# Optimization experiments

Measured on AMD Instinct MI355X. Metric: run time of the kernel, lower is better.

The kernel has to match this reference:

```python
import jax, jax.numpy as jnp
import numpy as np

MARGIN = 1.0


def setup_inputs() -> dict:
    key = jax.random.key(0)
    k1, k2, k3 = jax.random.split(key, 3)
    B, D, C = 16384, 256, 2000
    pred_embedding = jax.random.normal(k1, (B, D), dtype=jnp.float32)
    batch_label = jax.random.randint(k2, (B,), 0, C, dtype=jnp.int64)
    train_classes = jnp.arange(C, dtype=jnp.int64)
    train_sig = jax.random.normal(k3, (D, C), dtype=jnp.float32)
    return {
        "pred_embedding": pred_embedding,
        "batch_label": batch_label,
        "train_classes": train_classes,
        "train_sig": train_sig,
    }


def reference(pred_embedding, batch_label, train_classes, train_sig):
    # scores[j, k] = <pred_embedding[j], train_sig[:, train_classes[k]]>
    # Single GEMM replaces the per-pair dot-product loops.
    sig_cols = train_sig[:, train_classes]            # [D, C]
    scores = jnp.einsum("bd,dc->bc", pred_embedding, sig_cols)  # [B, C]
    # ground-truth class score per row: <XW_j, train_sig[:, y_j]>
    gt = jnp.einsum("bd,db->b", pred_embedding, train_sig[:, batch_label])  # [B]
    # exclude the class equal to the row label
    mask = (train_classes[None, :] != batch_label[:, None])  # [B, C] bool
    hinge = jnp.maximum(MARGIN + scores - gt[:, None], 0.0)
    loss = jnp.sum(jnp.where(mask, hinge, 0.0))
    return loss
```

## Files before the change

### kernel.cpp

```cpp
#include <hip/hip_runtime.h>

#define B_SZ 16384
#define D_SZ 256
#define C_SZ 2000
#define C_PAD 2048
#define MARGIN_F 1.0f
#define NBLK 1024

typedef float floatx16 __attribute__((ext_vector_type(16)));

__device__ inline void gld_lds16(const void* g, void* l) {
  __builtin_amdgcn_global_load_lds(
      (const __attribute__((address_space(1))) void*)g,
      (__attribute__((address_space(3))) void*)l, 16, 0, 0);
}


__device__ inline int2 pack8_fp8(const float* v) {
  int lo = __builtin_amdgcn_cvt_pk_fp8_f32(v[0], v[1], 0, false);
  lo = __builtin_amdgcn_cvt_pk_fp8_f32(v[2], v[3], lo, true);
  int hi = __builtin_amdgcn_cvt_pk_fp8_f32(v[4], v[5], 0, false);
  hi = __builtin_amdgcn_cvt_pk_fp8_f32(v[6], v[7], hi, true);
  return make_int2(lo, hi);
}
__device__ inline float rt_fp8(float x) {
  int p = __builtin_amdgcn_cvt_pk_fp8_f32(x, x, 0, false);
  return __builtin_amdgcn_cvt_f32_fp8(p, 0);
}
__device__ inline void unpack4_fp8(int w, float* o) {
  o[0] = __builtin_amdgcn_cvt_f32_fp8(w, 0);
  o[1] = __builtin_amdgcn_cvt_f32_fp8(w, 1);
  o[2] = __builtin_amdgcn_cvt_f32_fp8(w, 2);
  o[3] = __builtin_amdgcn_cvt_f32_fp8(w, 3);
}

__global__ __launch_bounds__(256) void sigq_kernel(
    const float* __restrict__ sig, char* __restrict__ sigq,
    float* __restrict__ out) {
  int t = blockIdx.x * 256 + threadIdx.x;
  if (t == 0) out[0] = 0.f;
  int ln = t & 63, ks = (t >> 6) & 15, ct = t >> 10;
  int col = ct * 32 + (ln & 31);
  int kb = ks * 16 + (ln >> 5) * 8;
  float v[8];
#pragma unroll
  for (int j = 0; j < 8; j++)
    v[j] = (col < C_SZ) ? sig[(size_t)(kb + j) * C_SZ + col] : 0.f;
  *(int2*)(sigq + (size_t)t * 8) = pack8_fp8(v);
}

__global__ __launch_bounds__(256) void prep_kernel(
    const float* __restrict__ pred, const char* __restrict__ sigq,
    const int* __restrict__ label, char* __restrict__ predq,
    float* __restrict__ gt) {
  __shared__ float ldsP[16][260];
  int bid = (int)blockIdx.x;
  int tid = threadIdx.x;
  int lane = tid & 63;
  int w = tid >> 6;
  int tile = bid >> 1;
  int rhi = (bid & 1) * 16;
#pragma unroll
  for (int it = 0; it < 4; it++) {
    int idx = it * 1024 + tid * 4;
    int r = idx >> 8, c = idx & 255;
    *(float4*)&ldsP[r][c] = *(const float4*)(pred + (size_t)(bid * 16 + r) * D_SZ + c);
  }
  __syncthreads();
#pragma unroll
  for (int it = 0; it < 2; it++) {
    int ch = it * 256 + tid;
    int ri = ch & 15;
    int ks = (ch >> 4) & 15;
    int khh = ch >> 8;
    int kb = ks * 16 + khh * 8;
    int ln = khh * 32 + rhi + ri;
    float v[8];
#pragma unroll
    for (int j = 0; j < 8; j++) v[j] = ldsP[ri][kb + j];
    *(int2*)(predq + ((size_t)(tile * 16 + ks) * 64 + ln) * 8) = pack8_fp8(v);
  }
  int l = lane & 31;
  int half = lane >> 5;
#pragma unroll
  for (int it = 0; it < 2; it++) {
    int r = w * 4 + it * 2 + half;
    int row = bid * 16 + r;
    int lbl = label[row];
    int ltile = lbl >> 5, l5 = lbl & 31;
    int ks = l >> 1, khh = l & 1;
    int2 p8 = *(const int2*)(sigq +
        (((size_t)(ltile * 16 + ks) * 64) + khh * 32 + l5) * 8);
    float sv[8];
    unpack4_fp8(p8.x, sv);
    unpack4_fp8(p8.y, sv + 4);
    float s = 0.f;
#pragma unroll
    for (int j = 0; j < 8; j++)
      s += rt_fp8(ldsP[r][l * 8 + j]) * sv[j];
#pragma unroll
    for (int off = 16; off > 0; off >>= 1) s += __shfl_down(s, off, 32);
    if (l == 0) gt[row] = s;
  }
}

__global__ __launch_bounds__(256) void mfma_fused_kernel(
    const char* __restrict__ predq, const char* __restrict__ sigq,
    const float* __restrict__ gt, float* __restrict__ out) {
  __shared__ char Bs[4096 * 8];
  __shared__ float gtl[256];
  __shared__ float red[4];
  int tid = threadIdx.x;
  int lane = tid & 63;
  int w = tid >> 6;
  int kh = lane >> 5, lm = lane & 31;
  int bid = (int)blockIdx.x;
  int i = bid >> 3;
  int rsb = (bid & 7) * 8 + (i & 7);
  int cg = i >> 3;

#pragma unroll
  for (int s = 0; s < 8; s++) {
    int q0 = s * 256 + w * 64;
    gld_lds16(sigq + ((size_t)cg * 2048 + q0 + lane) * 16, (void*)(Bs + (size_t)q0 * 16));
  }
  if (w == 0)
    gld_lds16((const char*)gt + (size_t)rsb * 1024 + (size_t)lane * 16, (void*)gtl);

  const char* abase0 = predq + (size_t)(rsb * 8 + w * 2) * 8192 + (size_t)lane * 8;
  long afr[16];
#pragma unroll
  for (int ks = 0; ks < 16; ks++)
    afr[ks] = *(const long*)(abase0 + (size_t)ks * 512);
  __syncthreads();

  float sum = 0.f;
#pragma unroll
  for (int rt = 0; rt < 2; rt++) {
    if (rt == 1) {
      const char* abase1 = abase0 + 8192;
#pragma unroll
      for (int ks = 0; ks < 16; ks++)
        afr[ks] = *(const long*)(abase1 + (size_t)ks * 512);
    }
#pragma unroll
    for (int ct = 0; ct < 4; ct++) {
      floatx16 acc = {};
      const char* bbase = Bs + (size_t)ct * 8192 + (size_t)lane * 8;
#pragma unroll
      for (int ks = 0; ks < 16; ks++) {
        long b = *(const long*)(bbase + (size_t)ks * 512);
        acc = __builtin_amdgcn_mfma_f32_32x32x16_fp8_fp8(afr[ks], b, acc, 0, 0, 0);
      }
      int col = cg * 128 + ct * 32 + lm;
      float keep = (col < C_SZ) ? 1.f : 0.f;
#pragma unroll
      for (int reg = 0; reg < 16; reg++) {
        int rl = (reg & 3) + 8 * (reg >> 2) + 4 * kh;
        float mg = MARGIN_F - gtl[w * 64 + rt * 32 + rl];
        sum += keep * fmaxf(acc[reg] + mg, 0.f);
      }
    }
  }
#pragma unroll
  for (int off = 32; off > 0; off >>= 1) sum += __shfl_down(sum, off, 64);
  if (lane == 0) red[w] = sum;
  __syncthreads();
  if (tid == 0)
    atomicAdd(out, red[0] + red[1] + red[2] + red[3]
                   - (float)B_SZ * MARGIN_F / (float)NBLK);
}

extern "C" void kernel_launch(void* const* d_in, const int* in_sizes, int n_in,
                              void* d_out, int out_size, void* d_ws, size_t ws_size,
                              hipStream_t stream) {
  const float* pred  = (const float*)d_in[0];
  const int*   label = (const int*)d_in[1];
  const float* sig   = (const float*)d_in[3];
  float* out = (float*)d_out;

  float* gt    = (float*)d_ws;
  char*  predq = (char*)d_ws + (128 << 10);
  char*  sigq  = (char*)d_ws + (128 << 10) + (4 << 20);

  sigq_kernel<<<256, 256, 0, stream>>>(sig, sigq, out);
  prep_kernel<<<1024, 256, 0, stream>>>(pred, sigq, label, predq, gt);
  mfma_fused_kernel<<<NBLK, 256, 0, stream>>>(predq, sigq, gt, out);
}
```

Measured before the change: 92.79 us.

## Merge quantization kernels and compute ground-truth scores via MFMA in GEMM kernel

Folds the signature quantization into the pred quantization kernel, which removes one launch, and drops the separate ground-truth dot-product pass. Each wave in the GEMM kernel now computes its rows' label scores with an extra MFMA sweep over the label-gathered sigq columns and writes the diagonal into LDS. This removes a kernel boundary and the gt buffer round trip. The cost is two extra MFMA chains and scattered global loads per wave. The A-fragment order is also rearranged so the second tile's fragments are reused first.

```diff
diff --git a/kernel.cpp b/kernel.cpp
--- a/kernel.cpp
+++ b/kernel.cpp
@@ -3,7 +3,6 @@
 #define B_SZ 16384
 #define D_SZ 256
 #define C_SZ 2000
-#define C_PAD 2048
 #define MARGIN_F 1.0f
 #define NBLK 1024
 
@@ -23,43 +22,29 @@
   hi = __builtin_amdgcn_cvt_pk_fp8_f32(v[6], v[7], hi, true);
   return make_int2(lo, hi);
 }
-__device__ inline float rt_fp8(float x) {
-  int p = __builtin_amdgcn_cvt_pk_fp8_f32(x, x, 0, false);
-  return __builtin_amdgcn_cvt_f32_fp8(p, 0);
-}
-__device__ inline void unpack4_fp8(int w, float* o) {
-  o[0] = __builtin_amdgcn_cvt_f32_fp8(w, 0);
-  o[1] = __builtin_amdgcn_cvt_f32_fp8(w, 1);
-  o[2] = __builtin_amdgcn_cvt_f32_fp8(w, 2);
-  o[3] = __builtin_amdgcn_cvt_f32_fp8(w, 3);
-}
 
-__global__ __launch_bounds__(256) void sigq_kernel(
-    const float* __restrict__ sig, char* __restrict__ sigq,
+__global__ __launch_bounds__(256) void quant_kernel(
+    const float* __restrict__ pred, const float* __restrict__ sig,
+    char* __restrict__ predq, char* __restrict__ sigq,
     float* __restrict__ out) {
-  int t = blockIdx.x * 256 + threadIdx.x;
-  if (t == 0) out[0] = 0.f;
-  int ln = t & 63, ks = (t >> 6) & 15, ct = t >> 10;
-  int col = ct * 32 + (ln & 31);
-  int kb = ks * 16 + (ln >> 5) * 8;
-  float v[8];
-#pragma unroll
-  for (int j = 0; j < 8; j++)
-    v[j] = (col < C_SZ) ? sig[(size_t)(kb + j) * C_SZ + col] : 0.f;
-  *(int2*)(sigq + (size_t)t * 8) = pack8_fp8(v);
-}
-
-__global__ __launch_bounds__(256) void prep_kernel(
-    const float* __restrict__ pred, const char* __restrict__ sigq,
-    const int* __restrict__ label, char* __restrict__ predq,
-    float* __restrict__ gt) {
   __shared__ float ldsP[16][260];
   int bid = (int)blockIdx.x;
   int tid = threadIdx.x;
-  int lane = tid & 63;
-  int w = tid >> 6;
-  int tile = bid >> 1;
-  int rhi = (bid & 1) * 16;
+
+  if (tid < 64) {
+    int t = bid * 64 + tid;
+    if (t == 0) out[0] = 0.f;
+    int ln = tid;
+    int ks = (t >> 6) & 15, ct = t >> 10;
+    int col = ct * 32 + (ln & 31);
+    int kb = ks * 16 + (ln >> 5) * 8;
+    float v[8];
+#pragma unroll
+    for (int j = 0; j < 8; j++)
+      v[j] = (col < C_SZ) ? sig[(size_t)(kb + j) * C_SZ + col] : 0.f;
+    *(int2*)(sigq + (size_t)t * 8) = pack8_fp8(v);
+  }
+
 #pragma unroll
   for (int it = 0; it < 4; it++) {
     int idx = it * 1024 + tid * 4;
@@ -67,6 +52,9 @@
     *(float4*)&ldsP[r][c] = *(const float4*)(pred + (size_t)(bid * 16 + r) * D_SZ + c);
   }
   __syncthreads();
+
+  int tile = bid >> 1;
+  int rhi = (bid & 1) * 16;
 #pragma unroll
   for (int it = 0; it < 2; it++) {
     int ch = it * 256 + tid;
@@ -80,33 +68,11 @@
     for (int j = 0; j < 8; j++) v[j] = ldsP[ri][kb + j];
     *(int2*)(predq + ((size_t)(tile * 16 + ks) * 64 + ln) * 8) = pack8_fp8(v);
   }
-  int l = lane & 31;
-  int half = lane >> 5;
-#pragma unroll
-  for (int it = 0; it < 2; it++) {
-    int r = w * 4 + it * 2 + half;
-    int row = bid * 16 + r;
-    int lbl = label[row];
-    int ltile = lbl >> 5, l5 = lbl & 31;
-    int ks = l >> 1, khh = l & 1;
-    int2 p8 = *(const int2*)(sigq +
-        (((size_t)(ltile * 16 + ks) * 64) + khh * 32 + l5) * 8);
-    float sv[8];
-    unpack4_fp8(p8.x, sv);
-    unpack4_fp8(p8.y, sv + 4);
-    float s = 0.f;
-#pragma unroll
-    for (int j = 0; j < 8; j++)
-      s += rt_fp8(ldsP[r][l * 8 + j]) * sv[j];
-#pragma unroll
-    for (int off = 16; off > 0; off >>= 1) s += __shfl_down(s, off, 32);
-    if (l == 0) gt[row] = s;
-  }
 }
 
 __global__ __launch_bounds__(256) void mfma_fused_kernel(
     const char* __restrict__ predq, const char* __restrict__ sigq,
-    const float* __restrict__ gt, float* __restrict__ out) {
+    const int* __restrict__ label, float* __restrict__ out) {
   __shared__ char Bs[4096 * 8];
   __shared__ float gtl[256];
   __shared__ float red[4];
@@ -124,24 +90,60 @@
     int q0 = s * 256 + w * 64;
     gld_lds16(sigq + ((size_t)cg * 2048 + q0 + lane) * 16, (void*)(Bs + (size_t)q0 * 16));
   }
-  if (w == 0)
-    gld_lds16((const char*)gt + (size_t)rsb * 1024 + (size_t)lane * 16, (void*)gtl);
 
-  const char* abase0 = predq + (size_t)(rsb * 8 + w * 2) * 8192 + (size_t)lane * 8;
+  int rowbase = rsb * 256 + w * 64;
+  int lbl0 = label[rowbase + lm];
+  int lbl1 = label[rowbase + 32 + lm];
+
+  const char* abase = predq + (size_t)(rsb * 8 + w * 2) * 8192 + (size_t)lane * 8;
   long afr[16];
+
 #pragma unroll
   for (int ks = 0; ks < 16; ks++)
-    afr[ks] = *(const long*)(abase0 + (size_t)ks * 512);
+    afr[ks] = *(const long*)(abase + (size_t)ks * 512);
+  {
+    floatx16 accl = {};
+    const char* cb = sigq + (size_t)(lbl0 >> 5) * 8192 + (size_t)kh * 256
+                          + (size_t)(lbl0 & 31) * 8;
+#pragma unroll
+    for (int ks = 0; ks < 16; ks++) {
+      long b = *(const long*)(cb + (size_t)ks * 512);
+      accl = __builtin_amdgcn_mfma_f32_32x32x16_fp8_fp8(afr[ks], b, accl, 0, 0, 0);
+    }
+#pragma unroll
+    for (int reg = 0; reg < 16; reg++) {
+      int rl = (reg & 3) + 8 * (reg >> 2) + 4 * kh;
+      if (rl == lm) gtl[w * 64 + lm] = accl[reg];
+    }
+  }
+#pragma unroll
+  for (int ks = 0; ks < 16; ks++)
+    afr[ks] = *(const long*)(abase + 8192 + (size_t)ks * 512);
+  {
+    floatx16 accl = {};
+    const char* cb = sigq + (size_t)(lbl1 >> 5) * 8192 + (size_t)kh * 256
+                          + (size_t)(lbl1 & 31) * 8;
+#pragma unroll
+    for (int ks = 0; ks < 16; ks++) {
+      long b = *(const long*)(cb + (size_t)ks * 512);
+      accl = __builtin_amdgcn_mfma_f32_32x32x16_fp8_fp8(afr[ks], b, accl, 0, 0, 0);
+    }
+#pragma unroll
+    for (int reg = 0; reg < 16; reg++) {
+      int rl = (reg & 3) + 8 * (reg >> 2) + 4 * kh;
+      if (rl == lm) gtl[w * 64 + 32 + lm] = accl[reg];
+    }
+  }
   __syncthreads();
 
   float sum = 0.f;
 #pragma unroll
-  for (int rt = 0; rt < 2; rt++) {
-    if (rt == 1) {
-      const char* abase1 = abase0 + 8192;
+  for (int p = 0; p < 2; p++) {
+    int rt = 1 - p;
+    if (p == 1) {
 #pragma unroll
       for (int ks = 0; ks < 16; ks++)
-        afr[ks] = *(const long*)(abase1 + (size_t)ks * 512);
+        afr[ks] = *(const long*)(abase + (size_t)ks * 512);
     }
 #pragma unroll
     for (int ct = 0; ct < 4; ct++) {
@@ -179,11 +181,9 @@
   const float* sig   = (const float*)d_in[3];
   float* out = (float*)d_out;
 
-  float* gt    = (float*)d_ws;
-  char*  predq = (char*)d_ws + (128 << 10);
-  char*  sigq  = (char*)d_ws + (128 << 10) + (4 << 20);
+  char* predq = (char*)d_ws + (128 << 10);
+  char* sigq  = (char*)d_ws + (128 << 10) + (4 << 20);
 
-  sigq_kernel<<<256, 256, 0, stream>>>(sig, sigq, out);
-  prep_kernel<<<1024, 256, 0, stream>>>(pred, sigq, label, predq, gt);
-  mfma_fused_kernel<<<NBLK, 256, 0, stream>>>(predq, sigq, gt, out);
+  quant_kernel<<<1024, 256, 0, stream>>>(pred, sig, predq, sigq, out);
+  mfma_fused_kernel<<<NBLK, 256, 0, stream>>>(predq, sigq, label, out);
 }
```

Result: slower. 107.4 us (+15.7%).

## Merge pred and sig quantization into one kernel, split gt into separate kernel

Applied to the files above, without the earlier changes.

The signature quantization and the prediction quantization now run in a single kernel: each block converts a 16-row slice of pred straight from global memory to fp8, with no LDS staging, and its first wavefront also quantizes part of sig. The ground-truth dot product moves to its own kernel, which reads pred rows directly from global memory. This removes the LDS round trip and the block-wide barrier from the prep step. It still launches three kernels, gt_kernel now re-reads pred, and only one wavefront per block does the sig work.

```diff
diff --git a/kernel.cpp b/kernel.cpp
--- a/kernel.cpp
+++ b/kernel.cpp
@@ -3,7 +3,6 @@
 #define B_SZ 16384
 #define D_SZ 256
 #define C_SZ 2000
-#define C_PAD 2048
 #define MARGIN_F 1.0f
 #define NBLK 1024
 
@@ -34,52 +33,47 @@
   o[3] = __builtin_amdgcn_cvt_f32_fp8(w, 3);
 }
 
-__global__ __launch_bounds__(256) void sigq_kernel(
-    const float* __restrict__ sig, char* __restrict__ sigq,
+__global__ __launch_bounds__(256) void quant_kernel(
+    const float* __restrict__ pred, const float* __restrict__ sig,
+    char* __restrict__ predq, char* __restrict__ sigq,
     float* __restrict__ out) {
-  int t = blockIdx.x * 256 + threadIdx.x;
-  if (t == 0) out[0] = 0.f;
-  int ln = t & 63, ks = (t >> 6) & 15, ct = t >> 10;
-  int col = ct * 32 + (ln & 31);
-  int kb = ks * 16 + (ln >> 5) * 8;
-  float v[8];
+  int bid = (int)blockIdx.x;
+  int tid = threadIdx.x;
+
+  if (tid < 64) {
+    int t = bid * 64 + tid;
+    if (t == 0) out[0] = 0.f;
+    int ln = tid;
+    int ks = (t >> 6) & 15, ct = t >> 10;
+    int col = ct * 32 + (ln & 31);
+    int kb = ks * 16 + (ln >> 5) * 8;
+    float v[8];
 #pragma unroll
-  for (int j = 0; j < 8; j++)
-    v[j] = (col < C_SZ) ? sig[(size_t)(kb + j) * C_SZ + col] : 0.f;
-  *(int2*)(sigq + (size_t)t * 8) = pack8_fp8(v);
+    for (int j = 0; j < 8; j++)
+      v[j] = (col < C_SZ) ? sig[(size_t)(kb + j) * C_SZ + col] : 0.f;
+    *(int2*)(sigq + (size_t)t * 8) = pack8_fp8(v);
+  }
+
+  int ri = tid & 15;
+  int ks = tid >> 4;
+  int tile = bid >> 1;
+  int rhi = (bid & 1) * 16;
+  const float4* p = (const float4*)(pred + (size_t)(bid * 16 + ri) * D_SZ + ks * 16);
+  float4 f0 = p[0], f1 = p[1], f2 = p[2], f3 = p[3];
+  float lo[8] = {f0.x, f0.y, f0.z, f0.w, f1.x, f1.y, f1.z, f1.w};
+  float hi[8] = {f2.x, f2.y, f2.z, f2.w, f3.x, f3.y, f3.z, f3.w};
+  size_t cbase = ((size_t)(tile * 16 + ks) * 64 + rhi + ri) * 8;
+  *(int2*)(predq + cbase)           = pack8_fp8(lo);
+  *(int2*)(predq + cbase + 32 * 8)  = pack8_fp8(hi);
 }
 
-__global__ __launch_bounds__(256) void prep_kernel(
+__global__ __launch_bounds__(256) void gt_kernel(
     const float* __restrict__ pred, const char* __restrict__ sigq,
-    const int* __restrict__ label, char* __restrict__ predq,
-    float* __restrict__ gt) {
-  __shared__ float ldsP[16][260];
+    const int* __restrict__ label, float* __restrict__ gt) {
   int bid = (int)blockIdx.x;
   int tid = threadIdx.x;
   int lane = tid & 63;
   int w = tid >> 6;
-  int tile = bid >> 1;
-  int rhi = (bid & 1) * 16;
-#pragma unroll
-  for (int it = 0; it < 4; it++) {
-    int idx = it * 1024 + tid * 4;
-    int r = idx >> 8, c = idx & 255;
-    *(float4*)&ldsP[r][c] = *(const float4*)(pred + (size_t)(bid * 16 + r) * D_SZ + c);
-  }
-  __syncthreads();
-#pragma unroll
-  for (int it = 0; it < 2; it++) {
-    int ch = it * 256 + tid;
-    int ri = ch & 15;
-    int ks = (ch >> 4) & 15;
-    int khh = ch >> 8;
-    int kb = ks * 16 + khh * 8;
-    int ln = khh * 32 + rhi + ri;
-    float v[8];
-#pragma unroll
-    for (int j = 0; j < 8; j++) v[j] = ldsP[ri][kb + j];
-    *(int2*)(predq + ((size_t)(tile * 16 + ks) * 64 + ln) * 8) = pack8_fp8(v);
-  }
   int l = lane & 31;
   int half = lane >> 5;
 #pragma unroll
@@ -94,10 +88,12 @@
     float sv[8];
     unpack4_fp8(p8.x, sv);
     unpack4_fp8(p8.y, sv + 4);
+    const float4* pr = (const float4*)(pred + (size_t)row * D_SZ + l * 8);
+    float4 a0 = pr[0], a1 = pr[1];
+    float pv[8] = {a0.x, a0.y, a0.z, a0.w, a1.x, a1.y, a1.z, a1.w};
     float s = 0.f;
 #pragma unroll
-    for (int j = 0; j < 8; j++)
-      s += rt_fp8(ldsP[r][l * 8 + j]) * sv[j];
+    for (int j = 0; j < 8; j++) s += rt_fp8(pv[j]) * sv[j];
 #pragma unroll
     for (int off = 16; off > 0; off >>= 1) s += __shfl_down(s, off, 32);
     if (l == 0) gt[row] = s;
@@ -183,7 +179,7 @@
   char*  predq = (char*)d_ws + (128 << 10);
   char*  sigq  = (char*)d_ws + (128 << 10) + (4 << 20);
 
-  sigq_kernel<<<256, 256, 0, stream>>>(sig, sigq, out);
-  prep_kernel<<<1024, 256, 0, stream>>>(pred, sigq, label, predq, gt);
+  quant_kernel<<<1024, 256, 0, stream>>>(pred, sig, predq, sigq, out);
+  gt_kernel<<<1024, 256, 0, stream>>>(pred, sigq, label, gt);
   mfma_fused_kernel<<<NBLK, 256, 0, stream>>>(predq, sigq, gt, out);
 }
```

New measurement: 94.51 us. Within noise of the previous version (+1.9%).
